# Kernel tuning notes

Hardware: AMD Instinct MI355X
Metric: run time of the kernel (lower is better)

The kernel has to match this reference:

```python
import jax, jax.numpy as jnp
import numpy as np

H = 2048
I = 8192
E = 8
EI = I // E  # expert_intermediate_size = 1024


def setup_inputs() -> dict:
    key = jax.random.key(0)
    k1, k2, k3 = jax.random.split(key, 3)
    B, N = 4, 4096
    x = jax.random.normal(k1, (B, N, H), dtype=jnp.float32)
    position_ids = jnp.arange(B * N, dtype=jnp.int64).reshape(B, N)
    gate_up_proj = 0.02 * jax.random.normal(k2, (E, H, EI * 2), dtype=jnp.float32)
    down_proj = 0.02 * jax.random.normal(k3, (E, EI, H), dtype=jnp.float32)
    return {"x": x, "position_ids": position_ids,
            "gate_up_proj": gate_up_proj, "down_proj": down_proj}


def reference(x, position_ids, gate_up_proj, down_proj):
    # x: [B,N,H]; position_ids: [B,N] (or [N]); expert = pos % E.
    B, N, Hdim = x.shape
    if position_ids.ndim == 1:
        position_ids = jnp.broadcast_to(position_ids[None, :], (B, N))
    eids = (position_ids % E).reshape(B * N)
    flat = x.reshape(B * N, Hdim)

    # Modulo routing is perfectly balanced (N % E == 0 with sequential ids),
    # so group tokens by expert (stable sort) and run dense per-expert GEMMs
    # instead of per-token gathered-weight bmm (same math, no weight blowup).
    T = B * N
    order = jnp.argsort(eids)          # stable in jax -> tokens grouped by expert
    xg = flat[order].reshape(E, T // E, Hdim)            # [E, T/E, H]
    gu = jnp.einsum('ebh,ehk->ebk', xg, gate_up_proj)    # [E, T/E, 2*EI]
    gate, up = gu[..., :EI], gu[..., EI:]
    inter = jax.nn.silu(gate) * up                       # [E, T/E, EI]
    outg = jnp.einsum('ebi,eih->ebh', inter, down_proj)  # [E, T/E, H]
    out = jnp.zeros((T, Hdim), dtype=x.dtype).at[order].set(outg.reshape(T, Hdim))
    return out.reshape(B, N, Hdim)
```

## Files before the change

kernel.cpp:

```cpp
#include <hip/hip_runtime.h>
#include <hip/hip_bf16.h>

typedef unsigned short u16;
typedef __attribute__((ext_vector_type(8))) short short8;
typedef __attribute__((ext_vector_type(8))) unsigned short u16x8;
typedef __attribute__((ext_vector_type(4))) float f32x4;

#define H_DIM 2048
#define EI_DIM 1024
#define NEXP 8

template <int V> struct IC { static constexpr int value = V; };

__device__ __forceinline__ u16 f2bf(float f) {
  __hip_bfloat16 h = __float2bfloat16(f);
  return __builtin_bit_cast(unsigned short, h);
}

__device__ __forceinline__ void load_lds16(const void* g, void* lds) {
  __builtin_amdgcn_global_load_lds(
      (const __attribute__((address_space(1))) unsigned int*)g,
      (__attribute__((address_space(3))) unsigned int*)lds, 16, 0, 0);
}

__global__ void hist_kernel(const int* __restrict__ pid, int* __restrict__ hist) {
  int seg = blockIdx.x, lane = threadIdx.x;
  int eid = pid[seg * 64 + lane] & 7;
#pragma unroll
  for (int e = 0; e < NEXP; ++e) {
    unsigned long long m = __ballot(eid == e);
    if (lane == 0) hist[e * 256 + seg] = __popcll(m);
  }
}

__global__ void scan_kernel(const int* __restrict__ hist, int* __restrict__ base,
                            int* __restrict__ offcnt, int T) {
  __shared__ int lds[256];
  int tid = threadIdx.x;
  int v[8], s = 0;
#pragma unroll
  for (int j = 0; j < 8; ++j) { v[j] = hist[tid * 8 + j]; s += v[j]; }
  lds[tid] = s;
  __syncthreads();
  for (int d = 1; d < 256; d <<= 1) {
    int t = (tid >= d) ? lds[tid - d] : 0;
    __syncthreads();
    lds[tid] += t;
    __syncthreads();
  }
  int run = lds[tid] - s;
#pragma unroll
  for (int j = 0; j < 8; ++j) { base[tid * 8 + j] = run; run += v[j]; }
  __syncthreads();
  if (tid < NEXP) {
    int o = base[tid * 256];
    int nx = (tid < NEXP - 1) ? base[(tid + 1) * 256] : T;
    offcnt[tid] = o;
    offcnt[8 + tid] = nx - o;
  }
}

__global__ void rank_kernel(const int* __restrict__ pid, const int* __restrict__ base,
                            int* __restrict__ order) {
  int seg = blockIdx.x, lane = threadIdx.x;
  int t = seg * 64 + lane;
  int eid = pid[t] & 7;
  unsigned long long below = (1ull << lane) - 1ull;
#pragma unroll
  for (int e = 0; e < NEXP; ++e) {
    unsigned long long m = __ballot(eid == e);
    if (eid == e) {
      int r = __popcll(m & below);
      order[base[e * 256 + seg] + r] = t;
    }
  }
}

__global__ __launch_bounds__(256) void transpose_bf16(const float* __restrict__ in,
                                                      u16* __restrict__ out, int R, int C) {
  __shared__ u16 tile[64][65];
  int nbr = R >> 6, nbc = C >> 6;
  int per_e = nbr * nbc;
  int bx = blockIdx.x;
  int e = bx / per_e, rem = bx % per_e;
  int tr = rem % nbr, tc = rem / nbr;
  const float* ine = in + (size_t)e * R * C;
  u16* oute = out + (size_t)e * R * C;
  int r0 = tr * 64, c0 = tc * 64;
  int tid = threadIdx.x;
  int lrow = tid >> 4, lc4 = (tid & 15) * 4;
#pragma unroll
  for (int p = 0; p < 4; ++p) {
    int rl = p * 16 + lrow;
    float4 v = *(const float4*)&ine[(size_t)(r0 + rl) * C + c0 + lc4];
    tile[rl][lc4 + 0] = f2bf(v.x);
    tile[rl][lc4 + 1] = f2bf(v.y);
    tile[rl][lc4 + 2] = f2bf(v.z);
    tile[rl][lc4 + 3] = f2bf(v.w);
  }
  __syncthreads();
#pragma unroll
  for (int q = 0; q < 16; ++q) {
    int idx = q * 256 + tid;
    int jr = idx >> 6, hc = idx & 63;
    oute[(size_t)(c0 + jr) * R + r0 + hc] = tile[hc][jr];
  }
}

__global__ __launch_bounds__(256) void gather_x(const float* __restrict__ x,
                                                const int* __restrict__ order,
                                                u16* __restrict__ xg) {
  int g = blockIdx.x;
  int t = order[g];
  const float* src = x + (size_t)t * H_DIM;
  u16* dst = xg + (size_t)g * H_DIM;
  int c = threadIdx.x * 8;
  float4 a = *(const float4*)&src[c];
  float4 b = *(const float4*)&src[c + 4];
  u16x8 v;
  v[0] = f2bf(a.x); v[1] = f2bf(a.y); v[2] = f2bf(a.z); v[3] = f2bf(a.w);
  v[4] = f2bf(b.x); v[5] = f2bf(b.y); v[6] = f2bf(b.z); v[7] = f2bf(b.w);
  *(u16x8*)&dst[c] = v;
}

template <int KTOT, int KIND>
__device__ __forceinline__ void gemm8_body(
    const u16* __restrict__ A, const u16* __restrict__ Bmat, void* __restrict__ outp,
    const int* __restrict__ offcnt, const int* __restrict__ order, int T) {
  constexpr int NK = KTOT / 64;
  constexpr int ASTR = (KIND == 0) ? H_DIM : EI_DIM;
  constexpr int BSTR = ASTR;
  constexpr size_t BEXP = (size_t)2048 * BSTR;
  __shared__ u16 As[2][2][8192];
  __shared__ u16 Bs[2][2][8192];

  int nwg = gridDim.x;
  int bid = blockIdx.x;
  int bx = (bid & 7) * (nwg >> 3) + (bid >> 3);
  int e = bx >> 6;
  int s = bx & 63;
  int off = offcnt[e], cnt = offcnt[8 + e];
  const u16* Be = Bmat + (size_t)e * BEXP;

  int tid = threadIdx.x, w = tid >> 6, l = tid & 63;
  int wm = w >> 2, wn = w & 3, lr = l & 15, lg = l >> 4;
  int cidx = (lg ^ ((lr >> 1) & 3)) * 8;
  int aRow0 = wm * 128 + lr;
  int bRow0 = wn * 64 + lr;
  int sr[2], sc[2];
#pragma unroll
  for (int j = 0; j < 2; ++j) {
    sr[j] = j * 128 + (tid >> 2);
    int c = tid & 3;
    sc[j] = (c ^ ((sr[j] >> 1) & 3)) * 8;
  }

#pragma unroll 1
  for (int it = s; it < 512; it += 64) {
    int mt = it >> 3, nt = it & 7;
    if (mt * 256 >= cnt) continue;

    const u16* aSrc[2];
    const u16* bSrc[2];
#pragma unroll
    for (int j = 0; j < 2; ++j) {
      int r = sr[j];
      int grow = min(off + mt * 256 + r, T - 1);
      aSrc[j] = A + (size_t)grow * ASTR + sc[j];
      int n;
      if (KIND == 0) {
        int q = r >> 4, rr = r & 15;
        n = ((q & 2) ? EI_DIM : 0) + nt * 128 + ((q >> 2) << 5) + ((q & 1) << 4) + rr;
      } else {
        n = nt * 256 + r;
      }
      bSrc[j] = Be + (size_t)n * BSTR + sc[j];
    }

    auto stageA = [&](int kt, int kh, int buf) {
#pragma unroll
      for (int j = 0; j < 2; ++j)
        load_lds16(aSrc[j] + kt * 64 + kh * 32, &As[buf][kh][j * 4096 + w * 512]);
    };
    auto stageB = [&](int kt, int kh, int buf) {
#pragma unroll
      for (int j = 0; j < 2; ++j)
        load_lds16(bSrc[j] + kt * 64 + kh * 32, &Bs[buf][kh][j * 4096 + w * 512]);
    };

    short8 avA[4], avB[4], bvA[4], bvB[4];
    auto RDA = [&](short8(&dst)[4], int buf, int kh, int h) {
#pragma unroll
      for (int mm = 0; mm < 4; ++mm)
        dst[mm] = *(const short8*)&As[buf][kh][(aRow0 + (h * 4 + mm) * 16) * 32 + cidx];
    };
    auto RDB = [&](short8(&dst)[4], int buf, int kh) {
#pragma unroll
      for (int nn = 0; nn < 4; ++nn)
        dst[nn] = *(const short8*)&Bs[buf][kh][(bRow0 + nn * 16) * 32 + cidx];
    };

    f32x4 acc[8][4];
#pragma unroll
    for (int m = 0; m < 8; ++m)
#pragma unroll
      for (int nn = 0; nn < 4; ++nn) acc[m][nn] = {0.f, 0.f, 0.f, 0.f};

    auto MF = [&](short8(&a)[4], short8(&b)[4], auto HC) {
      constexpr int h = decltype(HC)::value;
      __builtin_amdgcn_s_setprio(1);
#pragma unroll
      for (int mm = 0; mm < 4; ++mm)
#pragma unroll
        for (int nn = 0; nn < 4; ++nn)
          acc[h * 4 + mm][nn] =
              __builtin_amdgcn_mfma_f32_16x16x32_bf16(a[mm], b[nn], acc[h * 4 + mm][nn], 0, 0, 0);
      __builtin_amdgcn_s_setprio(0);
    };

    __syncthreads();

    stageA(0, 0, 0); stageB(0, 0, 0); stageA(0, 1, 0); stageB(0, 1, 0);
    stageB(1, 0, 1); stageA(1, 0, 1); stageB(1, 1, 1);
    asm volatile("s_waitcnt vmcnt(6)" ::: "memory");
    __builtin_amdgcn_s_barrier();
    __builtin_amdgcn_sched_barrier(0);

    auto TILE = [&](int t, auto BC) {
      constexpr int b = decltype(BC)::value;
      constexpr int bn = b ^ 1;
      RDA(avA, b, 0, 0);
      RDB(bvA, b, 0);
      stageA(t + 1, 1, bn);
      MF(avA, bvA, IC<0>{});
      RDA(avB, b, 0, 1);
      __builtin_amdgcn_s_barrier();
      stageB(t + 2, 0, b);
      MF(avB, bvA, IC<1>{});
      RDA(avA, b, 1, 0);
      RDB(bvB, b, 1);
      __builtin_amdgcn_s_barrier();
      stageA(t + 2, 0, b);
      MF(avA, bvB, IC<0>{});
      asm volatile("s_waitcnt vmcnt(4)" ::: "memory");
      RDA(avB, b, 1, 1);
      __builtin_amdgcn_s_barrier();
      stageB(t + 2, 1, b);
      MF(avB, bvB, IC<1>{});
      __builtin_amdgcn_s_barrier();
    };

#pragma unroll 1
    for (int t = 0; t < NK - 3; t += 2) {
      TILE(t, IC<0>{});
      TILE(t + 1, IC<1>{});
    }

    {
      RDA(avA, 0, 0, 0);
      RDB(bvA, 0, 0);
      stageA(NK - 1, 1, 1);
      MF(avA, bvA, IC<0>{});
      RDA(avB, 0, 0, 1);
      __builtin_amdgcn_s_barrier();
      MF(avB, bvA, IC<1>{});
      RDA(avA, 0, 1, 0);
      RDB(bvB, 0, 1);
      __builtin_amdgcn_s_barrier();
      MF(avA, bvB, IC<0>{});
      asm volatile("s_waitcnt vmcnt(0)" ::: "memory");
      RDA(avB, 0, 1, 1);
      __builtin_amdgcn_s_barrier();
      MF(avB, bvB, IC<1>{});
      __builtin_amdgcn_s_barrier();
      RDA(avA, 1, 0, 0);
      RDB(bvA, 1, 0);
      MF(avA, bvA, IC<0>{});
      RDA(avB, 1, 0, 1);
      MF(avB, bvA, IC<1>{});
      RDA(avA, 1, 1, 0);
      RDB(bvB, 1, 1);
      MF(avA, bvB, IC<0>{});
      RDA(avB, 1, 1, 1);
      MF(avB, bvB, IC<1>{});
    }

    if (KIND == 0) {
      u16* inter = (u16*)outp;
#pragma unroll
      for (int m = 0; m < 8; ++m)
#pragma unroll
        for (int nn = 0; nn < 2; ++nn) {
          f32x4 g = acc[m][nn], u = acc[m][nn + 2];
          int icol = nt * 128 + wn * 32 + nn * 16 + lr;
#pragma unroll
          for (int j = 0; j < 4; ++j) {
            int r = wm * 128 + m * 16 + lg * 4 + j;
            int grow = mt * 256 + r;
            if (grow < cnt) {
              float gv = g[j];
              float val = (gv / (1.f + __expf(-gv))) * u[j];
              inter[(size_t)(off + grow) * EI_DIM + icol] = f2bf(val);
            }
          }
        }
    } else {
      float* out = (float*)outp;
      float* lf = (float*)&As[0][0][0];
#pragma unroll
      for (int m = 0; m < 8; ++m) {
        __syncthreads();
#pragma unroll
        for (int nn = 0; nn < 4; ++nn)
#pragma unroll
          for (int j = 0; j < 4; ++j)
            lf[(wm * 16 + lg * 4 + j) * 256 + wn * 64 + nn * 16 + lr] = acc[m][nn][j];
        __syncthreads();
#pragma unroll
        for (int k = 0; k < 4; ++k) {
          int idx = tid + k * 512;
          int rl = idx >> 6, c4 = idx & 63;
          int grow = mt * 256 + (rl >> 4) * 128 + m * 16 + (rl & 15);
          if (grow < cnt) {
            int tt = order[off + grow];
            *(float4*)&out[(size_t)tt * H_DIM + nt * 256 + c4 * 4] =
                *(const float4*)&lf[rl * 256 + c4 * 4];
          }
        }
      }
    }
  }
}

__global__ __launch_bounds__(512, 2) void gemm_gu_kernel(
    const u16* __restrict__ A, const u16* __restrict__ Bmat, void* __restrict__ outp,
    const int* __restrict__ offcnt, int T) {
  gemm8_body<2048, 0>(A, Bmat, outp, offcnt, nullptr, T);
}

__global__ __launch_bounds__(512, 2) void gemm_down_kernel(
    const u16* __restrict__ A, const u16* __restrict__ Bmat, void* __restrict__ outp,
    const int* __restrict__ offcnt, const int* __restrict__ order, int T) {
  gemm8_body<1024, 1>(A, Bmat, outp, offcnt, order, T);
}

extern "C" void kernel_launch(void* const* d_in, const int* in_sizes, int n_in,
                              void* d_out, int out_size, void* d_ws, size_t ws_size,
                              hipStream_t stream) {
  const float* x = (const float*)d_in[0];
  const int* pid = (const int*)d_in[1];
  const float* gup = (const float*)d_in[2];
  const float* dwn = (const float*)d_in[3];
  float* out = (float*)d_out;

  const int T = in_sizes[1];

  char* ws = (char*)d_ws;
  size_t o = 0;
  auto take = [&](size_t b) { size_t r = o; o += (b + 255) & ~(size_t)255; return r; };
  int* offcnt = (int*)(ws + take(32 * 4));
  int* hist = (int*)(ws + take(2048 * 4));
  int* base = (int*)(ws + take(2052 * 4));
  int* order = (int*)(ws + take((size_t)T * 4));
  u16* xg = (u16*)(ws + take((size_t)T * H_DIM * 2));
  u16* wguT = (u16*)(ws + take((size_t)NEXP * 2048 * 2048 * 2));
  u16* wdT = (u16*)(ws + take((size_t)NEXP * 2048 * 1024 * 2));
  u16* inter = (u16*)(ws + take((size_t)T * EI_DIM * 2));

  hist_kernel<<<T / 64, 64, 0, stream>>>(pid, hist);
  scan_kernel<<<1, 256, 0, stream>>>(hist, base, offcnt, T);
  rank_kernel<<<T / 64, 64, 0, stream>>>(pid, base, order);
  transpose_bf16<<<NEXP * 32 * 32, 256, 0, stream>>>(gup, wguT, 2048, 2048);
  transpose_bf16<<<NEXP * 16 * 32, 256, 0, stream>>>(dwn, wdT, 1024, 2048);
  gather_x<<<T, 256, 0, stream>>>(x, order, xg);

  gemm_gu_kernel<<<512, 512, 0, stream>>>(xg, wguT, inter, offcnt, T);
  gemm_down_kernel<<<512, 512, 0, stream>>>(inter, wdT, out, offcnt, order, T);
}
```

Baseline: 333.1 us.

## Replace fine-grained interleaved staging with simple double-buffered prefetch loop

Replaces the hand-tuned pipeline, which interleaved half-tile global-to-LDS stages two tiles ahead between MFMA groups with several barriers per tile, with a plain double-buffer scheme. Each tile now issues all four stage loads for the next tile up front, computes on the current buffer, then waits for all loads and synchronises once. This cuts barriers and simplifies the schedule, but shortens the prefetch distance from two tiles to one and uses a full vmcnt(0) wait, so more memory latency may be exposed.

```diff
diff --git a/kernel.cpp b/kernel.cpp
--- a/kernel.cpp
+++ b/kernel.cpp
@@ -220,70 +220,43 @@
 
     __syncthreads();
 
-    stageA(0, 0, 0); stageB(0, 0, 0); stageA(0, 1, 0); stageB(0, 1, 0);
-    stageB(1, 0, 1); stageA(1, 0, 1); stageB(1, 1, 1);
-    asm volatile("s_waitcnt vmcnt(6)" ::: "memory");
+    stageA(0, 0, 0); stageA(0, 1, 0); stageB(0, 0, 0); stageB(0, 1, 0);
+    asm volatile("s_waitcnt vmcnt(0)" ::: "memory");
     __builtin_amdgcn_s_barrier();
-    __builtin_amdgcn_sched_barrier(0);
-
-    auto TILE = [&](int t, auto BC) {
+
+    auto TILE = [&](int t, auto BC, auto SC) {
       constexpr int b = decltype(BC)::value;
       constexpr int bn = b ^ 1;
+      constexpr bool stg = decltype(SC)::value;
+      if constexpr (stg) {
+        stageA(t + 1, 0, bn);
+        stageA(t + 1, 1, bn);
+        stageB(t + 1, 0, bn);
+        stageB(t + 1, 1, bn);
+      }
       RDA(avA, b, 0, 0);
       RDB(bvA, b, 0);
-      stageA(t + 1, 1, bn);
       MF(avA, bvA, IC<0>{});
       RDA(avB, b, 0, 1);
-      __builtin_amdgcn_s_barrier();
-      stageB(t + 2, 0, b);
       MF(avB, bvA, IC<1>{});
       RDA(avA, b, 1, 0);
       RDB(bvB, b, 1);
-      __builtin_amdgcn_s_barrier();
-      stageA(t + 2, 0, b);
       MF(avA, bvB, IC<0>{});
-      asm volatile("s_waitcnt vmcnt(4)" ::: "memory");
       RDA(avB, b, 1, 1);
-      __builtin_amdgcn_s_barrier();
-      stageB(t + 2, 1, b);
       MF(avB, bvB, IC<1>{});
-      __builtin_amdgcn_s_barrier();
+      if constexpr (stg) {
+        asm volatile("s_waitcnt vmcnt(0)" ::: "memory");
+        __builtin_amdgcn_s_barrier();
+      }
     };
 
 #pragma unroll 1
-    for (int t = 0; t < NK - 3; t += 2) {
-      TILE(t, IC<0>{});
-      TILE(t + 1, IC<1>{});
+    for (int t = 0; t < NK - 2; t += 2) {
+      TILE(t, IC<0>{}, IC<1>{});
+      TILE(t + 1, IC<1>{}, IC<1>{});
     }
-
-    {
-      RDA(avA, 0, 0, 0);
-      RDB(bvA, 0, 0);
-      stageA(NK - 1, 1, 1);
-      MF(avA, bvA, IC<0>{});
-      RDA(avB, 0, 0, 1);
-      __builtin_amdgcn_s_barrier();
-      MF(avB, bvA, IC<1>{});
-      RDA(avA, 0, 1, 0);
-      RDB(bvB, 0, 1);
-      __builtin_amdgcn_s_barrier();
-      MF(avA, bvB, IC<0>{});
-      asm volatile("s_waitcnt vmcnt(0)" ::: "memory");
-      RDA(avB, 0, 1, 1);
-      __builtin_amdgcn_s_barrier();
-      MF(avB, bvB, IC<1>{});
-      __builtin_amdgcn_s_barrier();
-      RDA(avA, 1, 0, 0);
-      RDB(bvA, 1, 0);
-      MF(avA, bvA, IC<0>{});
-      RDA(avB, 1, 0, 1);
-      MF(avB, bvA, IC<1>{});
-      RDA(avA, 1, 1, 0);
-      RDB(bvB, 1, 1);
-      MF(avA, bvB, IC<0>{});
-      RDA(avB, 1, 1, 1);
-      MF(avB, bvB, IC<1>{});
-    }
+    TILE(NK - 2, IC<0>{}, IC<1>{});
+    TILE(NK - 1, IC<1>{}, IC<0>{});
 
     if (KIND == 0) {
       u16* inter = (u16*)outp;
```

After: 349.4 us. 4.9% more time.
